# Optimization experiments

Measured on AMD Instinct MI355X. Metric: run time of the kernel, lower is better.

## Reference

```python
import jax, jax.numpy as jnp
import numpy as np


def setup_inputs() -> dict:
    key = jax.random.key(0)
    k1, k2, k3, k4 = jax.random.split(key, 4)
    M, K, N, G = 4, 8192, 28672, 128
    x = jax.random.normal(k1, (M, K), dtype=jnp.float16)
    # packed uint4 pairs stored as bytes (values 0..255); int32 carrier dtype
    weight_packed = jax.random.randint(k2, (K // 2, N), 0, 256, dtype=jnp.int32)
    # small positive scales, typical of int4 quant
    scales = (jax.random.uniform(k3, (K // G, N), dtype=jnp.float16) * 0.02 + 0.001).astype(jnp.float16)
    bias = jax.random.normal(k4, (N,), dtype=jnp.float16)
    return {"x": x, "weight_packed": weight_packed, "scales": scales, "bias": bias, "group_size": G}


def _dequant(weight_packed, scales, group_size):
    # weight_packed: [K//2, N] bytes; low nibble = even k, high nibble = odd k
    half_K, N = weight_packed.shape
    K = 2 * half_K
    low = weight_packed & 0xF
    high = (weight_packed >> 4) & 0xF
    w = jnp.stack([low, high], axis=1).reshape(K, N)  # interleave along K
    deq = w.astype(jnp.float16) - jnp.float16(8.0)     # symmetric int4, zero-point 8
    # per-group scale along K: scales is [K//group_size, N]
    deq = (deq.reshape(K // group_size, group_size, N) * scales[:, None, :]).reshape(K, N)
    return deq


def reference(x, weight_packed, scales, bias, group_size):
    deq = _dequant(weight_packed, scales, group_size)  # [K, N] fp16
    out = jnp.einsum('mk,kn->mn', x, deq, preferred_element_type=jnp.float32)
    out = out.astype(jnp.float16)
    return out + bias
```

## Files before the change

kernel.cpp:

```cpp
#include <hip/hip_runtime.h>
#include <stdint.h>

#define M_DIM 4
#define K_DIM 8192
#define N_DIM 28672
#define GRP 128
#define KK_PER_GRP (GRP / 2)
#define N_GROUPS (K_DIM / GRP)
#define BLOCK 256

#define CPT 8
#define COLS_PER_BLOCK (BLOCK * CPT)
#define NBLK_FAST (N_DIM / COLS_PER_BLOCK)
#define PF 4


__global__ __launch_bounds__(BLOCK, 4) void int4_gemv_fast(
    const float* __restrict__ x,
    const int*   __restrict__ wp,
    const float* __restrict__ scales,
    float*       __restrict__ ws)
{
    __shared__ float xs[GRP * M_DIM];

    const int tid = threadIdx.x;
    const int g   = blockIdx.y;
    const int n0  = blockIdx.x * COLS_PER_BLOCK + tid * CPT;

    #pragma unroll
    for (int e = tid; e < GRP * M_DIM; e += BLOCK) {
        const int m = e >> 7;
        const int j = e & 127;
        xs[j * M_DIM + m] = x[m * K_DIM + g * GRP + j];
    }
    __syncthreads();

    float acc[M_DIM][CPT];
    #pragma unroll
    for (int m = 0; m < M_DIM; m++)
        #pragma unroll
        for (int c = 0; c < CPT; c++) acc[m][c] = 0.f;

    const int* wrow = wp + (size_t)g * KK_PER_GRP * N_DIM + n0;

    int4 bufA[PF], bufB[PF];
    #pragma unroll
    for (int i = 0; i < PF; i++) {
        bufA[i] = *(const int4*)(wrow + (size_t)i * N_DIM);
        bufB[i] = *(const int4*)(wrow + (size_t)i * N_DIM + 4);
    }

    #pragma unroll 4
    for (int kk = 0; kk < KK_PER_GRP; kk++) {
        const int cur = kk & (PF - 1);
        const int4 wa = bufA[cur];
        const int4 wb = bufB[cur];
        if (kk + PF < KK_PER_GRP) {
            bufA[cur] = *(const int4*)(wrow + (size_t)(kk + PF) * N_DIM);
            bufB[cur] = *(const int4*)(wrow + (size_t)(kk + PF) * N_DIM + 4);
        }

        const float4 xlo = *(const float4*)&xs[(2 * kk) * M_DIM];
        const float4 xhi = *(const float4*)&xs[(2 * kk + 1) * M_DIM];

        const int wv[CPT] = {wa.x, wa.y, wa.z, wa.w, wb.x, wb.y, wb.z, wb.w};
        #pragma unroll
        for (int c = 0; c < CPT; c++) {
            const float lo = (float)(wv[c] & 0xF) - 8.0f;
            const float hi = (float)(wv[c] >> 4) - 8.0f;
            acc[0][c] = fmaf(xlo.x, lo, acc[0][c]);
            acc[1][c] = fmaf(xlo.y, lo, acc[1][c]);
            acc[2][c] = fmaf(xlo.z, lo, acc[2][c]);
            acc[3][c] = fmaf(xlo.w, lo, acc[3][c]);
            acc[0][c] = fmaf(xhi.x, hi, acc[0][c]);
            acc[1][c] = fmaf(xhi.y, hi, acc[1][c]);
            acc[2][c] = fmaf(xhi.z, hi, acc[2][c]);
            acc[3][c] = fmaf(xhi.w, hi, acc[3][c]);
        }
    }

    const float4 s0 = *(const float4*)(scales + (size_t)g * N_DIM + n0);
    const float4 s1 = *(const float4*)(scales + (size_t)g * N_DIM + n0 + 4);
    const float sc[CPT] = {s0.x, s0.y, s0.z, s0.w, s1.x, s1.y, s1.z, s1.w};

    float* wsp = ws + (size_t)g * (M_DIM * N_DIM);
    #pragma unroll
    for (int m = 0; m < M_DIM; m++) {
        float4 o0 = make_float4(acc[m][0] * sc[0], acc[m][1] * sc[1],
                                acc[m][2] * sc[2], acc[m][3] * sc[3]);
        float4 o1 = make_float4(acc[m][4] * sc[4], acc[m][5] * sc[5],
                                acc[m][6] * sc[6], acc[m][7] * sc[7]);
        *(float4*)(wsp + (size_t)m * N_DIM + n0)     = o0;
        *(float4*)(wsp + (size_t)m * N_DIM + n0 + 4) = o1;
    }
}

__global__ __launch_bounds__(256) void int4_gemv_reduce64(
    const float* __restrict__ ws,
    const float* __restrict__ bias,
    float*       __restrict__ out)
{
    const int mn = (blockIdx.x * 256 + threadIdx.x) * 4;
    if (mn >= M_DIM * N_DIM) return;
    const int n = mn % N_DIM;
    float4 a = *(const float4*)(bias + n);
    #pragma unroll 8
    for (int s = 0; s < N_GROUPS; s++) {
        const float4 v = *(const float4*)(ws + (size_t)s * (M_DIM * N_DIM) + mn);
        a.x += v.x; a.y += v.y; a.z += v.z; a.w += v.w;
    }
    *(float4*)(out + mn) = a;
}

#define G_CPT 4
#define G_COLS_PER_BLOCK (BLOCK * G_CPT)
#define G_NBLK (N_DIM / G_COLS_PER_BLOCK)

__global__ __launch_bounds__(BLOCK) void int4_gemv_generic(
    const float* __restrict__ x, const int* __restrict__ wp,
    const float* __restrict__ scales, float* __restrict__ ws, int gps)
{
    __shared__ float xs[GRP * M_DIM];
    const int tid = threadIdx.x;
    const int split = blockIdx.y;
    const int g0 = split * gps;
    const int n0 = blockIdx.x * G_COLS_PER_BLOCK + tid * G_CPT;

    float acc[M_DIM][G_CPT];
    #pragma unroll
    for (int m = 0; m < M_DIM; m++)
        #pragma unroll
        for (int c = 0; c < G_CPT; c++) acc[m][c] = 0.f;

    for (int gi = 0; gi < gps; gi++) {
        const int g = g0 + gi;
        __syncthreads();
        for (int e = tid; e < GRP * M_DIM; e += BLOCK) {
            const int m = e & 3, j = e >> 2;
            xs[e] = x[m * K_DIM + g * GRP + j];
        }
        __syncthreads();
        const float4 sv = *(const float4*)(scales + (size_t)g * N_DIM + n0);
        const float s[G_CPT] = {sv.x, sv.y, sv.z, sv.w};
        float accg[M_DIM][G_CPT];
        #pragma unroll
        for (int m = 0; m < M_DIM; m++)
            #pragma unroll
            for (int c = 0; c < G_CPT; c++) accg[m][c] = 0.f;
        const int* wrow = wp + (size_t)(g * KK_PER_GRP) * N_DIM + n0;
        #pragma unroll 4
        for (int kkl = 0; kkl < KK_PER_GRP; kkl++) {
            const int4 w4 = *(const int4*)(wrow + (size_t)kkl * N_DIM);
            float xl[M_DIM], xh[M_DIM];
            #pragma unroll
            for (int m = 0; m < M_DIM; m++) {
                xl[m] = xs[(2 * kkl) * M_DIM + m];
                xh[m] = xs[(2 * kkl + 1) * M_DIM + m];
            }
            const int wv[4] = {w4.x, w4.y, w4.z, w4.w};
            #pragma unroll
            for (int c = 0; c < G_CPT; c++) {
                const float lo = (float)(wv[c] & 0xF) - 8.0f;
                const float hi = (float)(wv[c] >> 4) - 8.0f;
                #pragma unroll
                for (int m = 0; m < M_DIM; m++) {
                    accg[m][c] = fmaf(xl[m], lo, accg[m][c]);
                    accg[m][c] = fmaf(xh[m], hi, accg[m][c]);
                }
            }
        }
        #pragma unroll
        for (int m = 0; m < M_DIM; m++)
            #pragma unroll
            for (int c = 0; c < G_CPT; c++)
                acc[m][c] = fmaf(accg[m][c], s[c], acc[m][c]);
    }
    float* wsp = ws + (size_t)split * (M_DIM * N_DIM);
    #pragma unroll
    for (int m = 0; m < M_DIM; m++)
        *(float4*)(wsp + (size_t)m * N_DIM + n0) =
            make_float4(acc[m][0], acc[m][1], acc[m][2], acc[m][3]);
}

__global__ __launch_bounds__(256) void int4_gemv_reduce_generic(
    const float* __restrict__ ws, const float* __restrict__ bias,
    float* __restrict__ out, int splits)
{
    const int idx = blockIdx.x * 256 + threadIdx.x;
    if (idx >= M_DIM * N_DIM) return;
    const int n = idx % N_DIM;
    float a = bias[n];
    for (int s = 0; s < splits; s++)
        a += ws[(size_t)s * (M_DIM * N_DIM) + idx];
    out[idx] = a;
}

extern "C" void kernel_launch(void* const* d_in, const int* in_sizes, int n_in,
                              void* d_out, int out_size, void* d_ws, size_t ws_size,
                              hipStream_t stream) {
    const float* x      = (const float*)d_in[0];
    const int*   wpk    = (const int*)d_in[1];
    const float* scales = (const float*)d_in[2];
    const float* bias   = (const float*)d_in[3];
    float* out = (float*)d_out;
    float* ws  = (float*)d_ws;

    const size_t need = (size_t)N_GROUPS * (M_DIM * N_DIM) * sizeof(float);
    if (ws_size >= need) {
        dim3 grid(NBLK_FAST, N_GROUPS);
        int4_gemv_fast<<<grid, BLOCK, 0, stream>>>(x, wpk, scales, ws);
        int4_gemv_reduce64<<<(M_DIM * N_DIM / 4 + 255) / 256, 256, 0, stream>>>(
            ws, bias, out);
    } else {
        int splits = N_GROUPS;
        while (splits > 1 &&
               (size_t)splits * (size_t)(M_DIM * N_DIM) * sizeof(float) > ws_size)
            splits >>= 1;
        const int gps = N_GROUPS / splits;
        dim3 grid(G_NBLK, splits);
        int4_gemv_generic<<<grid, BLOCK, 0, stream>>>(x, wpk, scales, ws, gps);
        int4_gemv_reduce_generic<<<(M_DIM * N_DIM + 255) / 256, 256, 0, stream>>>(
            ws, bias, out, splits);
    }
}
```

Measured before the change: 630.8 us.

## Split K into 128 slices with 16 columns per thread and nontemporal loads

Reworks the fast path so each block handles half a quantization group (32 packed rows) across 16 columns per thread, doubling the number of K splits to 128. Weight loads use nontemporal builtins with a two-stage register double buffer instead of a four-deep prefetch ring. This aims to increase memory-level parallelism per thread and avoid cache pollution from streaming weights. In exchange it doubles the partial-sum workspace the reduce kernel must write and read, and raises register pressure.

```diff
diff --git a/kernel.cpp b/kernel.cpp
--- a/kernel.cpp
+++ b/kernel.cpp
@@ -5,33 +5,40 @@
 #define K_DIM 8192
 #define N_DIM 28672
 #define GRP 128
-#define KK_PER_GRP (GRP / 2)
 #define N_GROUPS (K_DIM / GRP)
+#define SPLITS 128
+#define ROWS_PER_SPLIT 32
 #define BLOCK 256
 
-#define CPT 8
+#define CPT 16
 #define COLS_PER_BLOCK (BLOCK * CPT)
-#define NBLK_FAST (N_DIM / COLS_PER_BLOCK)
-#define PF 4
-
-
-__global__ __launch_bounds__(BLOCK, 4) void int4_gemv_fast(
+#define NBLK (N_DIM / COLS_PER_BLOCK)
+
+
+typedef int ivec4 __attribute__((ext_vector_type(4)));
+
+__device__ __forceinline__ ivec4 nt_load_iv4(const int* p) {
+    return __builtin_nontemporal_load((const ivec4*)p);
+}
+
+__global__ __launch_bounds__(BLOCK, 4) void int4_gemv_wide(
     const float* __restrict__ x,
     const int*   __restrict__ wp,
     const float* __restrict__ scales,
     float*       __restrict__ ws)
 {
-    __shared__ float xs[GRP * M_DIM];
+    __shared__ float xs[2 * ROWS_PER_SPLIT * M_DIM];
 
     const int tid = threadIdx.x;
-    const int g   = blockIdx.y;
+    const int sp  = blockIdx.y;
+    const int g   = sp >> 1;
+    const int k0  = sp * (2 * ROWS_PER_SPLIT);
     const int n0  = blockIdx.x * COLS_PER_BLOCK + tid * CPT;
 
-    #pragma unroll
-    for (int e = tid; e < GRP * M_DIM; e += BLOCK) {
-        const int m = e >> 7;
-        const int j = e & 127;
-        xs[j * M_DIM + m] = x[m * K_DIM + g * GRP + j];
+    {
+        const int m = tid >> 6;
+        const int j = tid & 63;
+        xs[j * M_DIM + m] = x[m * K_DIM + k0 + j];
     }
     __syncthreads();
 
@@ -41,61 +48,68 @@
         #pragma unroll
         for (int c = 0; c < CPT; c++) acc[m][c] = 0.f;
 
-    const int* wrow = wp + (size_t)g * KK_PER_GRP * N_DIM + n0;
-
-    int4 bufA[PF], bufB[PF];
-    #pragma unroll
-    for (int i = 0; i < PF; i++) {
-        bufA[i] = *(const int4*)(wrow + (size_t)i * N_DIM);
-        bufB[i] = *(const int4*)(wrow + (size_t)i * N_DIM + 4);
-    }
-
-    #pragma unroll 4
-    for (int kk = 0; kk < KK_PER_GRP; kk++) {
-        const int cur = kk & (PF - 1);
-        const int4 wa = bufA[cur];
-        const int4 wb = bufB[cur];
-        if (kk + PF < KK_PER_GRP) {
-            bufA[cur] = *(const int4*)(wrow + (size_t)(kk + PF) * N_DIM);
-            bufB[cur] = *(const int4*)(wrow + (size_t)(kk + PF) * N_DIM + 4);
-        }
-
-        const float4 xlo = *(const float4*)&xs[(2 * kk) * M_DIM];
-        const float4 xhi = *(const float4*)&xs[(2 * kk + 1) * M_DIM];
-
-        const int wv[CPT] = {wa.x, wa.y, wa.z, wa.w, wb.x, wb.y, wb.z, wb.w};
-        #pragma unroll
-        for (int c = 0; c < CPT; c++) {
-            const float lo = (float)(wv[c] & 0xF) - 8.0f;
-            const float hi = (float)(wv[c] >> 4) - 8.0f;
-            acc[0][c] = fmaf(xlo.x, lo, acc[0][c]);
-            acc[1][c] = fmaf(xlo.y, lo, acc[1][c]);
-            acc[2][c] = fmaf(xlo.z, lo, acc[2][c]);
-            acc[3][c] = fmaf(xlo.w, lo, acc[3][c]);
-            acc[0][c] = fmaf(xhi.x, hi, acc[0][c]);
-            acc[1][c] = fmaf(xhi.y, hi, acc[1][c]);
-            acc[2][c] = fmaf(xhi.z, hi, acc[2][c]);
-            acc[3][c] = fmaf(xhi.w, hi, acc[3][c]);
-        }
-    }
-
-    const float4 s0 = *(const float4*)(scales + (size_t)g * N_DIM + n0);
-    const float4 s1 = *(const float4*)(scales + (size_t)g * N_DIM + n0 + 4);
-    const float sc[CPT] = {s0.x, s0.y, s0.z, s0.w, s1.x, s1.y, s1.z, s1.w};
-
-    float* wsp = ws + (size_t)g * (M_DIM * N_DIM);
+    const int* wrow = wp + (size_t)(sp * ROWS_PER_SPLIT) * N_DIM + n0;
+
+    ivec4 buf[2][4];
+    #pragma unroll
+    for (int q = 0; q < 4; q++) buf[0][q] = nt_load_iv4(wrow + q * 4);
+
+    #pragma unroll 2
+    for (int r = 0; r < ROWS_PER_SPLIT; r++) {
+        const int cur = r & 1;
+        if (r + 1 < ROWS_PER_SPLIT) {
+            const int* nrow = wrow + (size_t)(r + 1) * N_DIM;
+            #pragma unroll
+            for (int q = 0; q < 4; q++) buf[cur ^ 1][q] = nt_load_iv4(nrow + q * 4);
+        }
+
+        const float4 xlo = *(const float4*)&xs[(2 * r) * M_DIM];
+        const float4 xhi = *(const float4*)&xs[(2 * r + 1) * M_DIM];
+
+        #pragma unroll
+        for (int q = 0; q < 4; q++) {
+            const ivec4 w4 = buf[cur][q];
+            #pragma unroll
+            for (int e = 0; e < 4; e++) {
+                const int c = q * 4 + e;
+                const int wb = w4[e];
+                const float lo = (float)(wb & 0xF) - 8.0f;
+                const float hi = (float)(wb >> 4) - 8.0f;
+                acc[0][c] = fmaf(xlo.x, lo, acc[0][c]);
+                acc[1][c] = fmaf(xlo.y, lo, acc[1][c]);
+                acc[2][c] = fmaf(xlo.z, lo, acc[2][c]);
+                acc[3][c] = fmaf(xlo.w, lo, acc[3][c]);
+                acc[0][c] = fmaf(xhi.x, hi, acc[0][c]);
+                acc[1][c] = fmaf(xhi.y, hi, acc[1][c]);
+                acc[2][c] = fmaf(xhi.z, hi, acc[2][c]);
+                acc[3][c] = fmaf(xhi.w, hi, acc[3][c]);
+            }
+        }
+    }
+
+    float sc[CPT];
+    #pragma unroll
+    for (int q = 0; q < 4; q++) {
+        const float4 s4 = *(const float4*)(scales + (size_t)g * N_DIM + n0 + q * 4);
+        sc[q * 4 + 0] = s4.x; sc[q * 4 + 1] = s4.y;
+        sc[q * 4 + 2] = s4.z; sc[q * 4 + 3] = s4.w;
+    }
+
+    float* wsp = ws + (size_t)sp * (M_DIM * N_DIM);
     #pragma unroll
     for (int m = 0; m < M_DIM; m++) {
-        float4 o0 = make_float4(acc[m][0] * sc[0], acc[m][1] * sc[1],
-                                acc[m][2] * sc[2], acc[m][3] * sc[3]);
-        float4 o1 = make_float4(acc[m][4] * sc[4], acc[m][5] * sc[5],
-                                acc[m][6] * sc[6], acc[m][7] * sc[7]);
-        *(float4*)(wsp + (size_t)m * N_DIM + n0)     = o0;
-        *(float4*)(wsp + (size_t)m * N_DIM + n0 + 4) = o1;
-    }
-}
-
-__global__ __launch_bounds__(256) void int4_gemv_reduce64(
+        #pragma unroll
+        for (int q = 0; q < 4; q++) {
+            float4 o = make_float4(acc[m][q * 4 + 0] * sc[q * 4 + 0],
+                                   acc[m][q * 4 + 1] * sc[q * 4 + 1],
+                                   acc[m][q * 4 + 2] * sc[q * 4 + 2],
+                                   acc[m][q * 4 + 3] * sc[q * 4 + 3]);
+            *(float4*)(wsp + (size_t)m * N_DIM + n0 + q * 4) = o;
+        }
+    }
+}
+
+__global__ __launch_bounds__(256) void int4_gemv_reduce128(
     const float* __restrict__ ws,
     const float* __restrict__ bias,
     float*       __restrict__ out)
@@ -105,7 +119,7 @@
     const int n = mn % N_DIM;
     float4 a = *(const float4*)(bias + n);
     #pragma unroll 8
-    for (int s = 0; s < N_GROUPS; s++) {
+    for (int s = 0; s < SPLITS; s++) {
         const float4 v = *(const float4*)(ws + (size_t)s * (M_DIM * N_DIM) + mn);
         a.x += v.x; a.y += v.y; a.z += v.z; a.w += v.w;
     }
@@ -115,6 +129,7 @@
 #define G_CPT 4
 #define G_COLS_PER_BLOCK (BLOCK * G_CPT)
 #define G_NBLK (N_DIM / G_COLS_PER_BLOCK)
+#define KK_PER_GRP (GRP / 2)
 
 __global__ __launch_bounds__(BLOCK) void int4_gemv_generic(
     const float* __restrict__ x, const int* __restrict__ wp,
@@ -205,11 +220,11 @@
     float* out = (float*)d_out;
     float* ws  = (float*)d_ws;
 
-    const size_t need = (size_t)N_GROUPS * (M_DIM * N_DIM) * sizeof(float);
+    const size_t need = (size_t)SPLITS * (M_DIM * N_DIM) * sizeof(float);
     if (ws_size >= need) {
-        dim3 grid(NBLK_FAST, N_GROUPS);
-        int4_gemv_fast<<<grid, BLOCK, 0, stream>>>(x, wpk, scales, ws);
-        int4_gemv_reduce64<<<(M_DIM * N_DIM / 4 + 255) / 256, 256, 0, stream>>>(
+        dim3 grid(NBLK, SPLITS);
+        int4_gemv_wide<<<grid, BLOCK, 0, stream>>>(x, wpk, scales, ws);
+        int4_gemv_reduce128<<<(M_DIM * N_DIM / 4 + 255) / 256, 256, 0, stream>>>(
             ws, bias, out);
     } else {
         int splits = N_GROUPS;
```

After: 668.0 us. 1.06x slower.
